# Kernel tuning notes

Measured on AMD Instinct MI355X. Metric: run time of the kernel, lower is better.

Reference implementation:

```python
import jax, jax.numpy as jnp
import numpy as np
import math

EPS_DEMOD = 1e-8
EPS_IN = 1e-5  # torch InstanceNorm2d default eps
STYLE_DIM = 512


def conv2d(x, w, pad, groups=1):
    return jax.lax.conv_general_dilated(
        x, w, window_strides=(1, 1), padding=[(pad, pad), (pad, pad)],
        dimension_numbers=('NCHW', 'OIHW', 'NCHW'), feature_group_count=groups)


def spade(x, seg, sw, sb, gw, gb, bw, bb):
    # param-free instance norm (biased variance, eps=1e-5)
    mu = jnp.mean(x, axis=(2, 3), keepdims=True)
    var = jnp.var(x, axis=(2, 3), keepdims=True)
    normalized = (x - mu) * jax.lax.rsqrt(var + EPS_IN)
    actv = jax.nn.relu(conv2d(seg, sw, 1) + sb[None, :, None, None])
    gamma = conv2d(actv, gw, 1) + gb[None, :, None, None]
    beta = conv2d(actv, bw, 1) + bb[None, :, None, None]
    return normalized * (1.0 + gamma) + beta


def modconv(x, style, w, mw, mb):
    # StyleGAN2 modulated/demodulated conv via grouped-conv trick (bias=False)
    B, I, H, W = x.shape
    O, _, k, _ = w.shape
    lin_scale = 1.0 / math.sqrt(STYLE_DIM)  # EqualLinear scale, lr_mul=1
    s = style @ (mw * lin_scale).T + mb  # [B, I]
    conv_scale = 1.0 / math.sqrt(I * k * k)
    weight = conv_scale * w[None] * s[:, None, :, None, None]  # [B,O,I,k,k]
    demod = jax.lax.rsqrt(jnp.sum(weight ** 2, axis=(2, 3, 4)) + EPS_DEMOD)
    weight = weight * demod[:, :, None, None, None]
    out = conv2d(x.reshape(1, B * I, H, W), weight.reshape(B * O, I, k, k),
                 pad=k // 2, groups=B)
    return out.reshape(B, O, H, W)


def lrelu(x):
    return jax.nn.leaky_relu(x, 0.2)


def setup_inputs() -> dict:
    key = jax.random.key(0)
    ks = jax.random.split(key, 32)
    B, FIN, FOUT, FMID, H, W = 8, 512, 256, 256, 64, 64
    SNC, NH, SD = 35, 128, STYLE_DIM
    i = iter(range(32))
    def n(k, shape):
        return jax.random.normal(k, shape, dtype=jnp.float32)
    inp = {}
    inp['x'] = n(ks[next(i)], (B, FIN, H, W))
    inp['seg'] = jax.random.uniform(ks[next(i)], (B, SNC, H, W), dtype=jnp.float32)
    inp['style'] = n(ks[next(i)], (B, SD))
    def spade_params(prefix, C):
        inp[prefix + '_sw'] = n(ks[next(i)], (NH, SNC, 3, 3)) * 0.05
        inp[prefix + '_sb'] = jnp.zeros((NH,), jnp.float32)
        inp[prefix + '_gw'] = n(ks[next(i)], (C, NH, 3, 3)) * 0.05
        inp[prefix + '_gb'] = jnp.zeros((C,), jnp.float32)
        inp[prefix + '_bw'] = n(ks[next(i)], (C, NH, 3, 3)) * 0.05
        inp[prefix + '_bb'] = jnp.zeros((C,), jnp.float32)
    spade_params('n0', FIN)
    spade_params('n1', FMID)
    spade_params('ns', FIN)
    # modulated convs: base weight ~ randn, modulation EqualLinear (bias_init=1)
    inp['w0'] = n(ks[next(i)], (FMID, FIN, 3, 3))
    inp['m0w'] = n(ks[next(i)], (FIN, SD))
    inp['m0b'] = jnp.ones((FIN,), jnp.float32)
    inp['w1'] = n(ks[next(i)], (FOUT, FMID, 3, 3))
    inp['m1w'] = n(ks[next(i)], (FMID, SD))
    inp['m1b'] = jnp.ones((FMID,), jnp.float32)
    inp['ws'] = n(ks[next(i)], (FOUT, FIN, 1, 1))
    inp['msw'] = n(ks[next(i)], (FIN, SD))
    inp['msb'] = jnp.ones((FIN,), jnp.float32)
    return inp


def reference(x, seg, style,
              n0_sw, n0_sb, n0_gw, n0_gb, n0_bw, n0_bb,
              n1_sw, n1_sb, n1_gw, n1_gb, n1_bw, n1_bb,
              ns_sw, ns_sb, ns_gw, ns_gb, ns_bw, ns_bb,
              w0, m0w, m0b, w1, m1w, m1b, ws, msw, msb):
    # shortcut: SPADE (no activation) -> 1x1 modulated conv
    x_s = modconv(spade(x, seg, ns_sw, ns_sb, ns_gw, ns_gb, ns_bw, ns_bb),
                  style, ws, msw, msb)
    dx = modconv(lrelu(spade(x, seg, n0_sw, n0_sb, n0_gw, n0_gb, n0_bw, n0_bb)),
                 style, w0, m0w, m0b)
    dx = modconv(lrelu(spade(dx, seg, n1_sw, n1_sb, n1_gw, n1_gb, n1_bw, n1_bb)),
                 style, w1, m1w, m1b)
    return x_s + dx
```

## Files before the change

### kernel.cpp

```cpp
#include <hip/hip_runtime.h>
#include <math.h>

#define BN 8
#define HW 4096
#define NH 128
#define SNC 35
#define SD 512

typedef __attribute__((ext_vector_type(8))) short short8v;
typedef __attribute__((ext_vector_type(4))) short short4v;
typedef __attribute__((ext_vector_type(4))) float float4v;
typedef __attribute__((ext_vector_type(4))) unsigned int uint4v;

__device__ __forceinline__ short f2bf(float f) {
  unsigned u = __float_as_uint(f);
  unsigned r = (u + 0x7fffu + ((u >> 16) & 1u)) >> 16;
  return (short)r;
}
__device__ __forceinline__ float bf2f(short h) {
  return __uint_as_float(((unsigned)(unsigned short)h) << 16);
}

__global__ __launch_bounds__(256) void stats_kernel(const float* __restrict__ x,
                                                    float* __restrict__ mu,
                                                    float* __restrict__ rstd) {
  int row = blockIdx.x;
  const float* p = x + (size_t)row * HW;
  float s = 0.f, s2 = 0.f;
  for (int i = threadIdx.x; i < HW; i += 256) {
    float v = p[i];
    s += v; s2 += v * v;
  }
  #pragma unroll
  for (int off = 32; off > 0; off >>= 1) {
    s  += __shfl_down(s, off);
    s2 += __shfl_down(s2, off);
  }
  __shared__ float as[4], as2[4];
  int wid = threadIdx.x >> 6;
  if ((threadIdx.x & 63) == 0) { as[wid] = s; as2[wid] = s2; }
  __syncthreads();
  if (threadIdx.x == 0) {
    float t  = as[0] + as[1] + as[2] + as[3];
    float t2 = as2[0] + as2[1] + as2[2] + as2[3];
    float m = t * (1.f / HW);
    float var = t2 * (1.f / HW) - m * m;
    mu[row] = m;
    rstd[row] = rsqrtf(var + 1e-5f);
  }
}

__global__ __launch_bounds__(256) void modscale_all_kernel(
    const float* __restrict__ style,
    const float* __restrict__ m0w, const float* __restrict__ m0b,
    const float* __restrict__ m1w, const float* __restrict__ m1b,
    const float* __restrict__ msw, const float* __restrict__ msb,
    float* __restrict__ s0, float* __restrict__ s1, float* __restrict__ ss) {
  int idx = blockIdx.x * 256 + threadIdx.x;
  const float *mw, *mb; float* o; int I;
  if (idx < 4096) { mw = m0w; mb = m0b; o = s0; I = 512; }
  else if (idx < 6144) { idx -= 4096; mw = m1w; mb = m1b; o = s1; I = 256; }
  else if (idx < 10240) { idx -= 6144; mw = msw; mb = msb; o = ss; I = 512; }
  else return;
  int b = idx / I, i = idx - b * I;
  const float* st = style + (size_t)b * SD;
  const float* w  = mw + (size_t)i * SD;
  float acc = 0.f;
  for (int d = 0; d < SD; ++d) acc += st[d] * w[d];
  o[idx] = acc * 0.044194173824159216f + mb[i];
}

__global__ __launch_bounds__(256) void wsq_all_kernel(
    const float* __restrict__ w0, const float* __restrict__ w1,
    const float* __restrict__ wss,
    float* __restrict__ wsq0, float* __restrict__ wsq1, float* __restrict__ wsqs) {
  int idx = blockIdx.x * 256 + threadIdx.x;
  const float* w; float* o; int KK;
  if (idx < 131072) { w = w0; o = wsq0; KK = 9; }
  else if (idx < 196608) { idx -= 131072; w = w1; o = wsq1; KK = 9; }
  else if (idx < 327680) { idx -= 196608; w = wss; o = wsqs; KK = 1; }
  else return;
  const float* p = w + (size_t)idx * KK;
  float a = 0.f;
  for (int t = 0; t < KK; ++t) a += p[t] * p[t];
  o[idx] = a;
}

__global__ __launch_bounds__(256) void demod_all_kernel(
    const float* __restrict__ wsq0, const float* __restrict__ s0, float* __restrict__ d0,
    const float* __restrict__ wsq1, const float* __restrict__ s1, float* __restrict__ d1,
    const float* __restrict__ wsqs, const float* __restrict__ ss, float* __restrict__ dss,
    float cs0, float cs1, float css) {
  int idx = blockIdx.x * 256 + threadIdx.x;
  const float *wsq, *s; float* dsc; int I; float cs;
  if (idx < 2048) { wsq = wsq0; s = s0; dsc = d0; I = 512; cs = cs0; }
  else if (idx < 4096) { idx -= 2048; wsq = wsq1; s = s1; dsc = d1; I = 256; cs = cs1; }
  else if (idx < 6144) { idx -= 4096; wsq = wsqs; s = ss; dsc = dss; I = 512; cs = css; }
  else return;
  int b = idx >> 8, o = idx & 255;
  const float* wr = wsq + (size_t)o * I;
  const float* sr = s + (size_t)b * I;
  float a = 0.f;
  for (int i = 0; i < I; ++i) { float sv = sr[i]; a += wr[i] * sv * sv; }
  dsc[idx] = rsqrtf(cs * cs * a + 1e-8f) * cs;
}

__device__ __forceinline__ void pack_one(int tid, const float* __restrict__ wg,
                                         const float* __restrict__ wb,
                                         short* __restrict__ ph, short* __restrict__ pl,
                                         int OCtot, int IC, int KK, int interleave) {
  int ICC = IC / 32;
  int OCT16 = OCtot / 16;
  int lane = tid & 63;
  int r = tid >> 6;
  int icC = r % ICC; r /= ICC;
  int ocT = r % OCT16; int tap = r / OCT16;
  int po = ocT * 16 + (lane & 15);
  int ic0 = icC * 32 + (lane >> 4) * 8;
  const float* srcw;
  int oc;
  if (interleave) { oc = po >> 1; srcw = (po & 1) ? wb : wg; }
  else { oc = po; srcw = wg; }
  short8v hv, lv;
  #pragma unroll
  for (int j = 0; j < 8; ++j) {
    float v = srcw[((size_t)oc * IC + ic0 + j) * KK + tap];
    short h = f2bf(v);
    hv[j] = h;
    lv[j] = f2bf(v - bf2f(h));
  }
  size_t o = (size_t)tid * 8;
  *(short8v*)(ph + o) = hv;
  if (pl) *(short8v*)(pl + o) = lv;
}

__global__ __launch_bounds__(256) void pack_w_all_kernel(
    const float* w0, const float* w1, const float* wss,
    const float* ns_gw, const float* ns_bw,
    const float* n0_gw, const float* n0_bw,
    const float* n1_gw, const float* n1_bw,
    short* p0h, short* p0l, short* p1h, short* p1l, short* psh, short* psl,
    short* pgsh, short* pg0h, short* pg1h) {
  int tid = blockIdx.x * 256 + threadIdx.x;
  if (tid < 147456) { pack_one(tid, w0, nullptr, p0h, p0l, 256, 512, 9, 0); return; }
  tid -= 147456;
  if (tid < 73728) { pack_one(tid, w1, nullptr, p1h, p1l, 256, 256, 9, 0); return; }
  tid -= 73728;
  if (tid < 16384) { pack_one(tid, wss, nullptr, psh, psl, 256, 512, 1, 0); return; }
  tid -= 16384;
  if (tid < 147456) { pack_one(tid, ns_gw, ns_bw, pgsh, nullptr, 1024, 128, 9, 1); return; }
  tid -= 147456;
  if (tid < 147456) { pack_one(tid, n0_gw, n0_bw, pg0h, nullptr, 1024, 128, 9, 1); return; }
  tid -= 147456;
  if (tid < 73728) pack_one(tid, n1_gw, n1_bw, pg1h, nullptr, 512, 128, 9, 1);
}

__global__ __launch_bounds__(256) void pack_sw_kernel(const float* __restrict__ sw0,
                                                      const float* __restrict__ sw1,
                                                      const float* __restrict__ sw2,
                                                      short* __restrict__ ph,
                                                      short* __restrict__ pl) {
  int tid = blockIdx.x * 256 + threadIdx.x;
  const int ICC = 2, OCT16 = 24;
  int total = 9 * OCT16 * ICC * 64;
  if (tid >= total) return;
  int lane = tid & 63;
  int r = tid >> 6;
  int icC = r % ICC; r /= ICC;
  int ocT = r % OCT16; int tap = r / OCT16;
  int oc = ocT * 16 + (lane & 15);
  int ic0 = icC * 32 + (lane >> 4) * 8;
  const float* srcw = (oc < 128) ? sw0 : ((oc < 256) ? sw1 : sw2);
  int ocl = oc & 127;
  short8v hv, lv;
  #pragma unroll
  for (int j = 0; j < 8; ++j) {
    int ic = ic0 + j;
    float v = (ic < SNC) ? srcw[((size_t)ocl * SNC + ic) * 9 + tap] : 0.f;
    short h = f2bf(v);
    hv[j] = h;
    lv[j] = f2bf(v - bf2f(h));
  }
  size_t o = (size_t)tid * 8;
  *(short8v*)(ph + o) = hv;
  *(short8v*)(pl + o) = lv;
}

__global__ __launch_bounds__(256) void seg_pack_kernel(const float* __restrict__ seg,
                                                       short* __restrict__ segT) {
  int pix = blockIdx.x * 256 + threadIdx.x;
  int b = pix >> 12, px = pix & 4095;
  float v[64];
  #pragma unroll
  for (int ic = 0; ic < SNC; ++ic)
    v[ic] = seg[((size_t)b * SNC + ic) * HW + px];
  #pragma unroll
  for (int ic = SNC; ic < 64; ++ic) v[ic] = 0.f;
  size_t o = (size_t)pix * 64;
  #pragma unroll
  for (int k = 0; k < 8; ++k) {
    short8v h;
    #pragma unroll
    for (int j = 0; j < 8; ++j) h[j] = f2bf(v[k * 8 + j]);
    *(short8v*)(segT + o + k * 8) = h;
  }
}

template<int IC, int ICSTRIDE, int K3, int MODE, int ACCUM, int INLO, int WLO>
__global__ __launch_bounds__(256) void conv_mfma_kernel(
    const short* __restrict__ in_hi, const short* __restrict__ in_lo,
    const short* __restrict__ wp_hi, const short* __restrict__ wp_lo,
    const float* __restrict__ dscale,
    const float* __restrict__ src, const float* __restrict__ mu,
    const float* __restrict__ rstd, const float* __restrict__ gbias,
    const float* __restrict__ bbias, const float* __restrict__ sscale,
    float* __restrict__ outF, short* __restrict__ out_hi,
    short* __restrict__ out_lo, int OCT16, int C, int icbase, int lrelu) {
  const int b = blockIdx.x;
  const int r0 = blockIdx.y * 2;
  const int zl = blockIdx.z;
  const int t = threadIdx.x;
  const int wv = t >> 6;
  const int lane = t & 63;
  const int l15 = lane & 15, lg = lane >> 4;
  const int ICC = IC / 32;
  const int PS = 2128;

  __shared__ __align__(16) short lds_hi[4 * 2128];
  __shared__ __align__(16) short lds_lo[INLO ? 4 * 2128 : 8];

  float pre[2][2][8];
  if (MODE == 1) {
    #pragma unroll
    for (int a = 0; a < 2; ++a) {
      int base = zl * 128 + wv * 32 + a * 16 + lg * 4;
      int cA = base >> 1, cB = cA + 1;
      const float* srcA = src + ((size_t)b * C + cA) * HW;
      const float* srcB = src + ((size_t)b * C + cB) * HW;
      #pragma unroll
      for (int pt = 0; pt < 8; ++pt) {
        int px = (r0 + (pt >> 2)) * 64 + (pt & 3) * 16 + l15;
        pre[a][0][pt] = srcA[px];
        pre[a][1][pt] = srcB[px];
      }
    }
  }

  float4v acc[2][8];
  #pragma unroll
  for (int a = 0; a < 2; ++a)
    #pragma unroll
    for (int pt = 0; pt < 8; ++pt) acc[a][pt] = (float4v){0.f, 0.f, 0.f, 0.f};

  for (int icC = 0; icC < ICC; ++icC) {
    __syncthreads();
    const int ic0 = icC * 32;
    for (int idx = t; idx < 264 * 4; idx += 256) {
      int pos = idx >> 2, part = idx & 3;
      int srow = pos / 66;
      int scol = pos - srow * 66;
      int gy = r0 + srow - 1, gx = scol - 1;
      uint4v vh = {0u, 0u, 0u, 0u}, vl = {0u, 0u, 0u, 0u};
      bool ok = (gy >= 0 && gy < 64 && gx >= 0 && gx < 64);
      if (!K3) ok = ok && (srow >= 1 && srow <= 2);
      if (ok) {
        size_t g = ((size_t)b * HW + gy * 64 + gx) * ICSTRIDE + icbase + ic0 + part * 8;
        vh = *(const uint4v*)(in_hi + g);
        if (INLO) vl = *(const uint4v*)(in_lo + g);
      }
      int lo = part * PS + pos * 8;
      *(uint4v*)(lds_hi + lo) = vh;
      if (INLO) *(uint4v*)(lds_lo + lo) = vl;
    }
    __syncthreads();

    if (K3) {
      #pragma unroll
      for (int dx = 0; dx < 3; ++dx) {
        short8v Ah[3][2], Al[3][2];
        #pragma unroll
        for (int dy = 0; dy < 3; ++dy) {
          #pragma unroll
          for (int a = 0; a < 2; ++a) {
            size_t wi = ((((size_t)(dy * 3 + dx) * OCT16) + (zl * 8 + wv * 2 + a)) * ICC + icC) * 64 + lane;
            Ah[dy][a] = *(const short8v*)(wp_hi + wi * 8);
            if (WLO) Al[dy][a] = *(const short8v*)(wp_lo + wi * 8);
          }
        }
        #pragma unroll
        for (int c0i = 0; c0i < 4; ++c0i) {
          #pragma unroll
          for (int sr = 0; sr < 4; ++sr) {
            int pix = sr * 66 + c0i * 16 + dx + l15;
            int addr = lg * PS + pix * 8;
            short8v Bh = *(const short8v*)(lds_hi + addr);
            #pragma unroll
            for (int dy = 0; dy < 3; ++dy) {
              int pt = sr - dy;
              if (pt < 0 || pt > 1) continue;
              int ptt = pt * 4 + c0i;
              acc[0][ptt] = __builtin_amdgcn_mfma_f32_16x16x32_bf16(Ah[dy][0], Bh, acc[0][ptt], 0, 0, 0);
              acc[1][ptt] = __builtin_amdgcn_mfma_f32_16x16x32_bf16(Ah[dy][1], Bh, acc[1][ptt], 0, 0, 0);
              if (WLO) {
                acc[0][ptt] = __builtin_amdgcn_mfma_f32_16x16x32_bf16(Al[dy][0], Bh, acc[0][ptt], 0, 0, 0);
                acc[1][ptt] = __builtin_amdgcn_mfma_f32_16x16x32_bf16(Al[dy][1], Bh, acc[1][ptt], 0, 0, 0);
              }
            }
            if (INLO) {
              short8v Bl = *(const short8v*)(lds_lo + addr);
              #pragma unroll
              for (int dy = 0; dy < 3; ++dy) {
                int pt = sr - dy;
                if (pt < 0 || pt > 1) continue;
                int ptt = pt * 4 + c0i;
                acc[0][ptt] = __builtin_amdgcn_mfma_f32_16x16x32_bf16(Ah[dy][0], Bl, acc[0][ptt], 0, 0, 0);
                acc[1][ptt] = __builtin_amdgcn_mfma_f32_16x16x32_bf16(Ah[dy][1], Bl, acc[1][ptt], 0, 0, 0);
              }
            }
          }
        }
      }
    } else {
      short8v Ah[2], Al[2];
      #pragma unroll
      for (int a = 0; a < 2; ++a) {
        size_t wi = (((size_t)(zl * 8 + wv * 2 + a)) * ICC + icC) * 64 + lane;
        Ah[a] = *(const short8v*)(wp_hi + wi * 8);
        if (WLO) Al[a] = *(const short8v*)(wp_lo + wi * 8);
      }
      #pragma unroll
      for (int pt = 0; pt < 8; ++pt) {
        int pix = ((pt >> 2) + 1) * 66 + (pt & 3) * 16 + 1 + l15;
        int addr = lg * PS + pix * 8;
        short8v Bh = *(const short8v*)(lds_hi + addr);
        acc[0][pt] = __builtin_amdgcn_mfma_f32_16x16x32_bf16(Ah[0], Bh, acc[0][pt], 0, 0, 0);
        acc[1][pt] = __builtin_amdgcn_mfma_f32_16x16x32_bf16(Ah[1], Bh, acc[1][pt], 0, 0, 0);
        if (WLO) {
          acc[0][pt] = __builtin_amdgcn_mfma_f32_16x16x32_bf16(Al[0], Bh, acc[0][pt], 0, 0, 0);
          acc[1][pt] = __builtin_amdgcn_mfma_f32_16x16x32_bf16(Al[1], Bh, acc[1][pt], 0, 0, 0);
        }
        if (INLO) {
          short8v Bl = *(const short8v*)(lds_lo + addr);
          acc[0][pt] = __builtin_amdgcn_mfma_f32_16x16x32_bf16(Ah[0], Bl, acc[0][pt], 0, 0, 0);
          acc[1][pt] = __builtin_amdgcn_mfma_f32_16x16x32_bf16(Ah[1], Bl, acc[1][pt], 0, 0, 0);
        }
      }
    }
  }

  if (MODE == 1) {
    #pragma unroll
    for (int a = 0; a < 2; ++a) {
      int base = zl * 128 + wv * 32 + a * 16 + lg * 4;
      int cA = base >> 1;
      int cB = cA + 1;
      float muA = mu[b * C + cA], rsA = rstd[b * C + cA];
      float gbA = gbias[cA], bbA = bbias[cA], sA = sscale[b * C + cA];
      float muB = mu[b * C + cB], rsB = rstd[b * C + cB];
      float gbB = gbias[cB], bbB = bbias[cB], sB = sscale[b * C + cB];
      #pragma unroll
      for (int pt = 0; pt < 8; ++pt) {
        int px = (r0 + (pt >> 2)) * 64 + (pt & 3) * 16 + l15;
        float nvA = (pre[a][0][pt] - muA) * rsA;
        float vA = nvA * (1.f + acc[a][pt][0] + gbA) + acc[a][pt][1] + bbA;
        if (lrelu) vA = (vA >= 0.f) ? vA : 0.2f * vA;
        vA *= sA;
        float nvB = (pre[a][1][pt] - muB) * rsB;
        float vB = nvB * (1.f + acc[a][pt][2] + gbB) + acc[a][pt][3] + bbB;
        if (lrelu) vB = (vB >= 0.f) ? vB : 0.2f * vB;
        vB *= sB;
        short hA = f2bf(vA), hB = f2bf(vB);
        short lA = f2bf(vA - bf2f(hA)), lB = f2bf(vB - bf2f(hB));
        size_t o = ((size_t)b * HW + px) * C + cA;
        *(unsigned*)(out_hi + o) =
            (unsigned)(unsigned short)hA | ((unsigned)(unsigned short)hB << 16);
        *(unsigned*)(out_lo + o) =
            (unsigned)(unsigned short)lA | ((unsigned)(unsigned short)lB << 16);
      }
    }
  } else if (MODE == 2) {
    #pragma unroll
    for (int a = 0; a < 2; ++a) {
      int ocbase = zl * 128 + wv * 32 + a * 16 + lg * 4;
      float bs[4];
      #pragma unroll
      for (int r = 0; r < 4; ++r) bs[r] = gbias[ocbase + r];
      #pragma unroll
      for (int pt = 0; pt < 8; ++pt) {
        int px = (r0 + (pt >> 2)) * 64 + (pt & 3) * 16 + l15;
        short4v hs;
        #pragma unroll
        for (int r = 0; r < 4; ++r)
          hs[r] = f2bf(fmaxf(acc[a][pt][r] + bs[r], 0.f));
        *(short4v*)(out_hi + ((size_t)b * HW + px) * C + ocbase) = hs;
      }
    }
  } else {
    #pragma unroll
    for (int a = 0; a < 2; ++a) {
      int ocbase = zl * 128 + wv * 32 + a * 16 + lg * 4;
      float ds[4];
      #pragma unroll
      for (int r = 0; r < 4; ++r) ds[r] = dscale[b * 256 + ocbase + r];
      #pragma unroll
      for (int pt = 0; pt < 8; ++pt) {
        int px = (r0 + (pt >> 2)) * 64 + (pt & 3) * 16 + l15;
        #pragma unroll
        for (int r = 0; r < 4; ++r) {
          size_t oi = ((size_t)b * 256 + ocbase + r) * HW + px;
          float v = acc[a][pt][r] * ds[r];
          if (ACCUM) v += outF[oi];
          outF[oi] = v;
        }
      }
    }
  }
}

__global__ __launch_bounds__(256) void conv_gb_dual_kernel(
    const short* __restrict__ actv_hi,
    const short* __restrict__ pgsh, const short* __restrict__ pg0h,
    const float* __restrict__ x, const float* __restrict__ mu,
    const float* __restrict__ rstd,
    const float* __restrict__ ns_gb, const float* __restrict__ ns_bb,
    const float* __restrict__ ss,
    const float* __restrict__ n0_gb, const float* __restrict__ n0_bb,
    const float* __restrict__ s0,
    short* __restrict__ sp2_hi, short* __restrict__ sp_hi) {
  const int b = blockIdx.x;
  const int r0 = blockIdx.y * 2;
  const int zz = blockIdx.z;
  const bool isN0 = zz >= 8;
  const int zl = zz & 7;
  const short* wph = isN0 ? pg0h : pgsh;
  const float* gbias = isN0 ? n0_gb : ns_gb;
  const float* bbias = isN0 ? n0_bb : ns_bb;
  const float* sscale = isN0 ? s0 : ss;
  short* out_hi = isN0 ? sp_hi : sp2_hi;
  const int icbase = isN0 ? 0 : 256;
  const int lrelu = isN0 ? 1 : 0;
  const int OCT16 = 64, C = 512, ICC = 4, ICSTRIDE = 384;

  const int t = threadIdx.x;
  const int wv = t >> 6;
  const int lane = t & 63;
  const int l15 = lane & 15, lg = lane >> 4;
  const int PS = 2128;

  __shared__ __align__(16) short lds_hi[16 * 2128];

  float pre[2][2][8];
  #pragma unroll
  for (int a = 0; a < 2; ++a) {
    int base = zl * 128 + wv * 32 + a * 16 + lg * 4;
    int cA = base >> 1, cB = cA + 1;
    const float* srcA = x + ((size_t)b * C + cA) * HW;
    const float* srcB = x + ((size_t)b * C + cB) * HW;
    #pragma unroll
    for (int pt = 0; pt < 8; ++pt) {
      int px = (r0 + (pt >> 2)) * 64 + (pt & 3) * 16 + l15;
      pre[a][0][pt] = srcA[px];
      pre[a][1][pt] = srcB[px];
    }
  }

  float4v acc[2][8];
  #pragma unroll
  for (int a = 0; a < 2; ++a)
    #pragma unroll
    for (int pt = 0; pt < 8; ++pt) acc[a][pt] = (float4v){0.f, 0.f, 0.f, 0.f};

  for (int idx = t; idx < 264 * 16; idx += 256) {
    int pos = idx >> 4, part = idx & 15;
    int srow = pos / 66;
    int scol = pos - srow * 66;
    int gy = r0 + srow - 1, gx = scol - 1;
    uint4v vh = {0u, 0u, 0u, 0u};
    if (gy >= 0 && gy < 64 && gx >= 0 && gx < 64)
      vh = *(const uint4v*)(actv_hi + ((size_t)b * HW + gy * 64 + gx) * ICSTRIDE
                            + icbase + part * 8);
    *(uint4v*)(lds_hi + part * PS + pos * 8) = vh;
  }
  __syncthreads();

  #pragma unroll
  for (int icC = 0; icC < 4; ++icC) {
    #pragma unroll
    for (int dx = 0; dx < 3; ++dx) {
      short8v Ah[3][2];
      #pragma unroll
      for (int dy = 0; dy < 3; ++dy) {
        #pragma unroll
        for (int a = 0; a < 2; ++a) {
          size_t wi = ((((size_t)(dy * 3 + dx) * OCT16) + (zl * 8 + wv * 2 + a)) * ICC + icC) * 64 + lane;
          Ah[dy][a] = *(const short8v*)(wph + wi * 8);
        }
      }
      #pragma unroll
      for (int c0i = 0; c0i < 4; ++c0i) {
        #pragma unroll
        for (int sr = 0; sr < 4; ++sr) {
          int pix = sr * 66 + c0i * 16 + dx + l15;
          int addr = (icC * 4 + lg) * PS + pix * 8;
          short8v Bh = *(const short8v*)(lds_hi + addr);
          #pragma unroll
          for (int dy = 0; dy < 3; ++dy) {
            int pt = sr - dy;
            if (pt < 0 || pt > 1) continue;
            int ptt = pt * 4 + c0i;
            acc[0][ptt] = __builtin_amdgcn_mfma_f32_16x16x32_bf16(Ah[dy][0], Bh, acc[0][ptt], 0, 0, 0);
            acc[1][ptt] = __builtin_amdgcn_mfma_f32_16x16x32_bf16(Ah[dy][1], Bh, acc[1][ptt], 0, 0, 0);
          }
        }
      }
    }
  }

  #pragma unroll
  for (int a = 0; a < 2; ++a) {
    int base = zl * 128 + wv * 32 + a * 16 + lg * 4;
    int cA = base >> 1;
    int cB = cA + 1;
    float muA = mu[b * C + cA], rsA = rstd[b * C + cA];
    float gbA = gbias[cA], bbA = bbias[cA], sA = sscale[b * C + cA];
    float muB = mu[b * C + cB], rsB = rstd[b * C + cB];
    float gbB = gbias[cB], bbB = bbias[cB], sB = sscale[b * C + cB];
    #pragma unroll
    for (int pt = 0; pt < 8; ++pt) {
      int px = (r0 + (pt >> 2)) * 64 + (pt & 3) * 16 + l15;
      float nvA = (pre[a][0][pt] - muA) * rsA;
      float vA = nvA * (1.f + acc[a][pt][0] + gbA) + acc[a][pt][1] + bbA;
      if (lrelu) vA = (vA >= 0.f) ? vA : 0.2f * vA;
      vA *= sA;
      float nvB = (pre[a][1][pt] - muB) * rsB;
      float vB = nvB * (1.f + acc[a][pt][2] + gbB) + acc[a][pt][3] + bbB;
      if (lrelu) vB = (vB >= 0.f) ? vB : 0.2f * vB;
      vB *= sB;
      short hA = f2bf(vA), hB = f2bf(vB);
      size_t o = ((size_t)b * HW + px) * C + cA;
      *(unsigned*)(out_hi + o) =
          (unsigned)(unsigned short)hA | ((unsigned)(unsigned short)hB << 16);
    }
  }
}

__global__ __launch_bounds__(256, 4) void conv_mc_dual_kernel(
    const short* __restrict__ sp_hi,
    const short* __restrict__ p0h, const short* __restrict__ p0l,
    const float* __restrict__ d0, float* __restrict__ bufH,
    const short* __restrict__ sp2_hi,
    const short* __restrict__ psh, const short* __restrict__ psl,
    const float* __restrict__ dss, float* __restrict__ outD) {
  const int b = blockIdx.x;
  const int r0 = blockIdx.y * 2;
  const int zz = blockIdx.z;
  const bool is1x1 = zz >= 2;
  const int zl = zz & 1;
  const int OCT16 = 16, ICC = 16, ICSTRIDE = 512;

  const int t = threadIdx.x;
  const int wv = t >> 6;
  const int lane = t & 63;
  const int l15 = lane & 15, lg = lane >> 4;
  const int PS = 2128;

  __shared__ __align__(16) short lds[8 * 2128];

  float4v acc[2][8];
  #pragma unroll
  for (int a = 0; a < 2; ++a)
    #pragma unroll
    for (int pt = 0; pt < 8; ++pt) acc[a][pt] = (float4v){0.f, 0.f, 0.f, 0.f};

  if (!is1x1) {
    for (int rnd = 0; rnd < 8; ++rnd) {
      __syncthreads();
      for (int idx = t; idx < 264 * 8; idx += 256) {
        int pos = idx >> 3, part = idx & 7;
        int srow = pos / 66;
        int scol = pos - srow * 66;
        int gy = r0 + srow - 1, gx = scol - 1;
        uint4v vh = {0u, 0u, 0u, 0u};
        if (gy >= 0 && gy < 64 && gx >= 0 && gx < 64)
          vh = *(const uint4v*)(sp_hi + ((size_t)b * HW + gy * 64 + gx) * ICSTRIDE
                                + rnd * 64 + part * 8);
        *(uint4v*)(lds + part * PS + pos * 8) = vh;
      }
      __syncthreads();

      #pragma unroll
      for (int sub = 0; sub < 2; ++sub) {
        const int icC = rnd * 2 + sub;
        #pragma unroll
        for (int dx = 0; dx < 3; ++dx) {
          short8v Ah[3][2], Al[3][2];
          #pragma unroll
          for (int dy = 0; dy < 3; ++dy) {
            #pragma unroll
            for (int a = 0; a < 2; ++a) {
              size_t wi = ((((size_t)(dy * 3 + dx) * OCT16) + (zl * 8 + wv * 2 + a)) * ICC + icC) * 64 + lane;
              Ah[dy][a] = *(const short8v*)(p0h + wi * 8);
              Al[dy][a] = *(const short8v*)(p0l + wi * 8);
            }
          }
          #pragma unroll
          for (int c0i = 0; c0i < 4; ++c0i) {
            #pragma unroll
            for (int sr = 0; sr < 4; ++sr) {
              int pix = sr * 66 + c0i * 16 + dx + l15;
              int addr = (sub * 4 + lg) * PS + pix * 8;
              short8v Bh = *(const short8v*)(lds + addr);
              #pragma unroll
              for (int dy = 0; dy < 3; ++dy) {
                int pt = sr - dy;
                if (pt < 0 || pt > 1) continue;
                int ptt = pt * 4 + c0i;
                acc[0][ptt] = __builtin_amdgcn_mfma_f32_16x16x32_bf16(Ah[dy][0], Bh, acc[0][ptt], 0, 0, 0);
                acc[1][ptt] = __builtin_amdgcn_mfma_f32_16x16x32_bf16(Ah[dy][1], Bh, acc[1][ptt], 0, 0, 0);
                acc[0][ptt] = __builtin_amdgcn_mfma_f32_16x16x32_bf16(Al[dy][0], Bh, acc[0][ptt], 0, 0, 0);
                acc[1][ptt] = __builtin_amdgcn_mfma_f32_16x16x32_bf16(Al[dy][1], Bh, acc[1][ptt], 0, 0, 0);
              }
            }
          }
        }
      }
    }
  } else {
    for (int icC = 0; icC < ICC; ++icC) {
      __syncthreads();
      const int ic0 = icC * 32;
      for (int idx = t; idx < 132 * 4; idx += 256) {
        int pos = idx >> 2, part = idx & 3;
        int srow = pos / 66;
        int scol = pos - srow * 66;
        int gy = r0 + srow, gx = scol - 1;
        uint4v vh = {0u, 0u, 0u, 0u};
        if (gx >= 0 && gx < 64)
          vh = *(const uint4v*)(sp2_hi + ((size_t)b * HW + gy * 64 + gx) * ICSTRIDE + ic0 + part * 8);
        *(uint4v*)(lds + part * PS + pos * 8) = vh;
      }
      __syncthreads();

      short8v Ah[2], Al[2];
      #pragma unroll
      for (int a = 0; a < 2; ++a) {
        size_t wi = (((size_t)(zl * 8 + wv * 2 + a)) * ICC + icC) * 64 + lane;
        Ah[a] = *(const short8v*)(psh + wi * 8);
        Al[a] = *(const short8v*)(psl + wi * 8);
      }
      #pragma unroll
      for (int pt = 0; pt < 8; ++pt) {
        int pix = (pt >> 2) * 66 + (pt & 3) * 16 + 1 + l15;
        short8v Bh = *(const short8v*)(lds + lg * PS + pix * 8);
        acc[0][pt] = __builtin_amdgcn_mfma_f32_16x16x32_bf16(Ah[0], Bh, acc[0][pt], 0, 0, 0);
        acc[1][pt] = __builtin_amdgcn_mfma_f32_16x16x32_bf16(Ah[1], Bh, acc[1][pt], 0, 0, 0);
        acc[0][pt] = __builtin_amdgcn_mfma_f32_16x16x32_bf16(Al[0], Bh, acc[0][pt], 0, 0, 0);
        acc[1][pt] = __builtin_amdgcn_mfma_f32_16x16x32_bf16(Al[1], Bh, acc[1][pt], 0, 0, 0);
      }
    }
  }

  const float* dscale = is1x1 ? dss : d0;
  float* outF = is1x1 ? outD : bufH;
  #pragma unroll
  for (int a = 0; a < 2; ++a) {
    int ocbase = zl * 128 + wv * 32 + a * 16 + lg * 4;
    float ds[4];
    #pragma unroll
    for (int r = 0; r < 4; ++r) ds[r] = dscale[b * 256 + ocbase + r];
    #pragma unroll
    for (int pt = 0; pt < 8; ++pt) {
      int px = (r0 + (pt >> 2)) * 64 + (pt & 3) * 16 + l15;
      #pragma unroll
      for (int r = 0; r < 4; ++r) {
        size_t oi = ((size_t)b * 256 + ocbase + r) * HW + px;
        outF[oi] = acc[a][pt][r] * ds[r];
      }
    }
  }
}

extern "C" void kernel_launch(void* const* d_in, const int* in_sizes, int n_in,
                              void* d_out, int out_size, void* d_ws, size_t ws_size,
                              hipStream_t stream) {
  const float* x     = (const float*)d_in[0];
  const float* seg   = (const float*)d_in[1];
  const float* style = (const float*)d_in[2];
  const float* n0_sw = (const float*)d_in[3];
  const float* n0_sb = (const float*)d_in[4];
  const float* n0_gw = (const float*)d_in[5];
  const float* n0_gb = (const float*)d_in[6];
  const float* n0_bw = (const float*)d_in[7];
  const float* n0_bb = (const float*)d_in[8];
  const float* n1_sw = (const float*)d_in[9];
  const float* n1_sb = (const float*)d_in[10];
  const float* n1_gw = (const float*)d_in[11];
  const float* n1_gb = (const float*)d_in[12];
  const float* n1_bw = (const float*)d_in[13];
  const float* n1_bb = (const float*)d_in[14];
  const float* ns_sw = (const float*)d_in[15];
  const float* ns_sb = (const float*)d_in[16];
  const float* ns_gw = (const float*)d_in[17];
  const float* ns_gb = (const float*)d_in[18];
  const float* ns_bw = (const float*)d_in[19];
  const float* ns_bb = (const float*)d_in[20];
  const float* w0  = (const float*)d_in[21];
  const float* m0w = (const float*)d_in[22];
  const float* m0b = (const float*)d_in[23];
  const float* w1  = (const float*)d_in[24];
  const float* m1w = (const float*)d_in[25];
  const float* m1b = (const float*)d_in[26];
  const float* wss = (const float*)d_in[27];
  const float* msw = (const float*)d_in[28];
  const float* msb = (const float*)d_in[29];
  float* out = (float*)d_out;

  char* p = (char*)d_ws;
  auto allocF = [&](size_t n) { float* r = (float*)p; p += n * 4; return r; };
  auto allocS = [&](size_t n) { short* r = (short*)p; p += n * 2; return r; };

  float* mu_x   = allocF(4096);
  float* rstd_x = allocF(4096);
  float* mu_h   = allocF(2048);
  float* rstd_h = allocF(2048);
  float* s0  = allocF(4096);
  float* s1  = allocF(2048);
  float* ss  = allocF(4096);
  float* d0  = allocF(2048);
  float* d1  = allocF(2048);
  float* dss = allocF(2048);
  float* wsq0 = allocF(256 * 512);
  float* wsq1 = allocF(256 * 256);
  float* wsqs = allocF(256 * 512);
  float* sb_cat = allocF(384);
  float* bufH = allocF((size_t)BN * 256 * HW);
  short* actv_hi = allocS((size_t)BN * HW * 384);
  short* segT = allocS((size_t)BN * HW * 64);
  short* sp_hi = allocS((size_t)BN * HW * 512);
  short* sp_lo = allocS((size_t)BN * HW * 512);
  short* sp2_hi = allocS((size_t)BN * HW * 512);
  short* p0h = allocS((size_t)256 * 512 * 9);
  short* p0l = allocS((size_t)256 * 512 * 9);
  short* p1h = allocS((size_t)256 * 256 * 9);
  short* p1l = allocS((size_t)256 * 256 * 9);
  short* psh = allocS((size_t)256 * 512);
  short* psl = allocS((size_t)256 * 512);
  short* pswh = allocS((size_t)9 * 24 * 2 * 64 * 8);
  short* pswl = allocS((size_t)9 * 24 * 2 * 64 * 8);
  short* pgsh = allocS((size_t)1024 * 128 * 9);
  short* pg0h = allocS((size_t)1024 * 128 * 9);
  short* pg1h = allocS((size_t)512 * 128 * 9);

  float cs0 = 1.0f / sqrtf(512.f * 9.f);
  float cs1 = 1.0f / sqrtf(256.f * 9.f);
  float css = 1.0f / sqrtf(512.f);

  stats_kernel<<<BN * 512, 256, 0, stream>>>(x, mu_x, rstd_x);
  modscale_all_kernel<<<40, 256, 0, stream>>>(style, m0w, m0b, m1w, m1b, msw, msb,
                                              s0, s1, ss);
  wsq_all_kernel<<<1280, 256, 0, stream>>>(w0, w1, wss, wsq0, wsq1, wsqs);
  demod_all_kernel<<<24, 256, 0, stream>>>(wsq0, s0, d0, wsq1, s1, d1, wsqs, ss, dss,
                                           cs0, cs1, css);

  seg_pack_kernel<<<(BN * HW) / 256, 256, 0, stream>>>(seg, segT);
  hipMemcpyAsync(sb_cat,       n0_sb, 128 * 4, hipMemcpyDeviceToDevice, stream);
  hipMemcpyAsync(sb_cat + 128, n1_sb, 128 * 4, hipMemcpyDeviceToDevice, stream);
  hipMemcpyAsync(sb_cat + 256, ns_sb, 128 * 4, hipMemcpyDeviceToDevice, stream);

  pack_sw_kernel<<<108, 256, 0, stream>>>(n0_sw, n1_sw, ns_sw, pswh, pswl);
  pack_w_all_kernel<<<2368, 256, 0, stream>>>(
      w0, w1, wss, ns_gw, ns_bw, n0_gw, n0_bw, n1_gw, n1_bw,
      p0h, p0l, p1h, p1l, psh, psl, pgsh, pg0h, pg1h);

  conv_mfma_kernel<64, 64, 1, 2, 0, 0, 1><<<dim3(BN, 32, 3), 256, 0, stream>>>(
      segT, nullptr, pswh, pswl, nullptr, nullptr, nullptr, nullptr, sb_cat,
      nullptr, nullptr, nullptr, actv_hi, nullptr, 24, 384, 0, 0);

  conv_gb_dual_kernel<<<dim3(BN, 32, 16), 256, 0, stream>>>(
      actv_hi, pgsh, pg0h, x, mu_x, rstd_x,
      ns_gb, ns_bb, ss, n0_gb, n0_bb, s0, sp2_hi, sp_hi);

  conv_mc_dual_kernel<<<dim3(BN, 32, 4), 256, 0, stream>>>(
      sp_hi, p0h, p0l, d0, bufH,
      sp2_hi, psh, psl, dss, out);

  stats_kernel<<<BN * 256, 256, 0, stream>>>(bufH, mu_h, rstd_h);
  conv_mfma_kernel<128, 384, 1, 1, 0, 0, 0><<<dim3(BN, 32, 4), 256, 0, stream>>>(
      actv_hi, nullptr, pg1h, nullptr, nullptr, bufH, mu_h, rstd_h, n1_gb, n1_bb, s1,
      nullptr, sp_hi, sp_lo, 32, 256, 128, 1);
  conv_mfma_kernel<256, 256, 1, 0, 1, 1, 1><<<dim3(BN, 32, 2), 256, 0, stream>>>(
      sp_hi, sp_lo, p1h, p1l, d1, nullptr, nullptr, nullptr, nullptr, nullptr,
      nullptr, out, nullptr, nullptr, 16, 0, 0, 0);
}
```

Measured before the change: 699.9 us.

## Drop low-bf16 weight split for conv0 and add dedicated single-stage gamma/beta conv kernel

Removes the low-part bf16 weight correction for the w0 modulated conv, which halves the MFMA count and weight loads in the largest conv. It also replaces the generic MODE==1 path of conv_mfma_kernel with a specialized conv_gb1_kernel. That kernel stages all 128 input channels into shared memory at once and reuses each LDS B-fragment across the three dy taps. The trade-offs are lower precision in the w0 conv, which could exceed the error tolerance, and heavier LDS use per block in the new kernel, which may reduce occupancy.

```diff
diff --git a/kernel.cpp b/kernel.cpp
--- a/kernel.cpp
+++ b/kernel.cpp
@@ -139,10 +139,10 @@
     const float* ns_gw, const float* ns_bw,
     const float* n0_gw, const float* n0_bw,
     const float* n1_gw, const float* n1_bw,
-    short* p0h, short* p0l, short* p1h, short* p1l, short* psh, short* psl,
+    short* p0h, short* p1h, short* p1l, short* psh, short* psl,
     short* pgsh, short* pg0h, short* pg1h) {
   int tid = blockIdx.x * 256 + threadIdx.x;
-  if (tid < 147456) { pack_one(tid, w0, nullptr, p0h, p0l, 256, 512, 9, 0); return; }
+  if (tid < 147456) { pack_one(tid, w0, nullptr, p0h, nullptr, 256, 512, 9, 0); return; }
   tid -= 147456;
   if (tid < 73728) { pack_one(tid, w1, nullptr, p1h, p1l, 256, 256, 9, 0); return; }
   tid -= 73728;
@@ -228,23 +228,6 @@
 
   __shared__ __align__(16) short lds_hi[4 * 2128];
   __shared__ __align__(16) short lds_lo[INLO ? 4 * 2128 : 8];
-
-  float pre[2][2][8];
-  if (MODE == 1) {
-    #pragma unroll
-    for (int a = 0; a < 2; ++a) {
-      int base = zl * 128 + wv * 32 + a * 16 + lg * 4;
-      int cA = base >> 1, cB = cA + 1;
-      const float* srcA = src + ((size_t)b * C + cA) * HW;
-      const float* srcB = src + ((size_t)b * C + cB) * HW;
-      #pragma unroll
-      for (int pt = 0; pt < 8; ++pt) {
-        int px = (r0 + (pt >> 2)) * 64 + (pt & 3) * 16 + l15;
-        pre[a][0][pt] = srcA[px];
-        pre[a][1][pt] = srcB[px];
-      }
-    }
-  }
 
   float4v acc[2][8];
   #pragma unroll
@@ -348,37 +331,7 @@
     }
   }
 
-  if (MODE == 1) {
-    #pragma unroll
-    for (int a = 0; a < 2; ++a) {
-      int base = zl * 128 + wv * 32 + a * 16 + lg * 4;
-      int cA = base >> 1;
-      int cB = cA + 1;
-      float muA = mu[b * C + cA], rsA = rstd[b * C + cA];
-      float gbA = gbias[cA], bbA = bbias[cA], sA = sscale[b * C + cA];
-      float muB = mu[b * C + cB], rsB = rstd[b * C + cB];
-      float gbB = gbias[cB], bbB = bbias[cB], sB = sscale[b * C + cB];
-      #pragma unroll
-      for (int pt = 0; pt < 8; ++pt) {
-        int px = (r0 + (pt >> 2)) * 64 + (pt & 3) * 16 + l15;
-        float nvA = (pre[a][0][pt] - muA) * rsA;
-        float vA = nvA * (1.f + acc[a][pt][0] + gbA) + acc[a][pt][1] + bbA;
-        if (lrelu) vA = (vA >= 0.f) ? vA : 0.2f * vA;
-        vA *= sA;
-        float nvB = (pre[a][1][pt] - muB) * rsB;
-        float vB = nvB * (1.f + acc[a][pt][2] + gbB) + acc[a][pt][3] + bbB;
-        if (lrelu) vB = (vB >= 0.f) ? vB : 0.2f * vB;
-        vB *= sB;
-        short hA = f2bf(vA), hB = f2bf(vB);
-        short lA = f2bf(vA - bf2f(hA)), lB = f2bf(vB - bf2f(hB));
-        size_t o = ((size_t)b * HW + px) * C + cA;
-        *(unsigned*)(out_hi + o) =
-            (unsigned)(unsigned short)hA | ((unsigned)(unsigned short)hB << 16);
-        *(unsigned*)(out_lo + o) =
-            (unsigned)(unsigned short)lA | ((unsigned)(unsigned short)lB << 16);
-      }
-    }
-  } else if (MODE == 2) {
+  if (MODE == 2) {
     #pragma unroll
     for (int a = 0; a < 2; ++a) {
       int ocbase = zl * 128 + wv * 32 + a * 16 + lg * 4;
@@ -544,9 +497,127 @@
   }
 }
 
+__global__ __launch_bounds__(256) void conv_gb1_kernel(
+    const short* __restrict__ actv_hi, const short* __restrict__ pg1h,
+    const float* __restrict__ src, const float* __restrict__ mu,
+    const float* __restrict__ rstd,
+    const float* __restrict__ gbias, const float* __restrict__ bbias,
+    const float* __restrict__ sscale,
+    short* __restrict__ out_hi, short* __restrict__ out_lo) {
+  const int b = blockIdx.x;
+  const int r0 = blockIdx.y * 2;
+  const int zl = blockIdx.z;
+  const int OCT16 = 32, C = 256, ICC = 4, ICSTRIDE = 384, icbase = 128;
+
+  const int t = threadIdx.x;
+  const int wv = t >> 6;
+  const int lane = t & 63;
+  const int l15 = lane & 15, lg = lane >> 4;
+  const int PS = 2128;
+
+  __shared__ __align__(16) short lds_hi[16 * 2128];
+
+  float pre[2][2][8];
+  #pragma unroll
+  for (int a = 0; a < 2; ++a) {
+    int base = zl * 128 + wv * 32 + a * 16 + lg * 4;
+    int cA = base >> 1, cB = cA + 1;
+    const float* srcA = src + ((size_t)b * C + cA) * HW;
+    const float* srcB = src + ((size_t)b * C + cB) * HW;
+    #pragma unroll
+    for (int pt = 0; pt < 8; ++pt) {
+      int px = (r0 + (pt >> 2)) * 64 + (pt & 3) * 16 + l15;
+      pre[a][0][pt] = srcA[px];
+      pre[a][1][pt] = srcB[px];
+    }
+  }
+
+  float4v acc[2][8];
+  #pragma unroll
+  for (int a = 0; a < 2; ++a)
+    #pragma unroll
+    for (int pt = 0; pt < 8; ++pt) acc[a][pt] = (float4v){0.f, 0.f, 0.f, 0.f};
+
+  for (int idx = t; idx < 264 * 16; idx += 256) {
+    int pos = idx >> 4, part = idx & 15;
+    int srow = pos / 66;
+    int scol = pos - srow * 66;
+    int gy = r0 + srow - 1, gx = scol - 1;
+    uint4v vh = {0u, 0u, 0u, 0u};
+    if (gy >= 0 && gy < 64 && gx >= 0 && gx < 64)
+      vh = *(const uint4v*)(actv_hi + ((size_t)b * HW + gy * 64 + gx) * ICSTRIDE
+                            + icbase + part * 8);
+    *(uint4v*)(lds_hi + part * PS + pos * 8) = vh;
+  }
+  __syncthreads();
+
+  #pragma unroll
+  for (int icC = 0; icC < 4; ++icC) {
+    #pragma unroll
+    for (int dx = 0; dx < 3; ++dx) {
+      short8v Ah[3][2];
+      #pragma unroll
+      for (int dy = 0; dy < 3; ++dy) {
+        #pragma unroll
+        for (int a = 0; a < 2; ++a) {
+          size_t wi = ((((size_t)(dy * 3 + dx) * OCT16) + (zl * 8 + wv * 2 + a)) * ICC + icC) * 64 + lane;
+          Ah[dy][a] = *(const short8v*)(pg1h + wi * 8);
+        }
+      }
+      #pragma unroll
+      for (int c0i = 0; c0i < 4; ++c0i) {
+        #pragma unroll
+        for (int sr = 0; sr < 4; ++sr) {
+          int pix = sr * 66 + c0i * 16 + dx + l15;
+          int addr = (icC * 4 + lg) * PS + pix * 8;
+          short8v Bh = *(const short8v*)(lds_hi + addr);
+          #pragma unroll
+          for (int dy = 0; dy < 3; ++dy) {
+            int pt = sr - dy;
+            if (pt < 0 || pt > 1) continue;
+            int ptt = pt * 4 + c0i;
+            acc[0][ptt] = __builtin_amdgcn_mfma_f32_16x16x32_bf16(Ah[dy][0], Bh, acc[0][ptt], 0, 0, 0);
+            acc[1][ptt] = __builtin_amdgcn_mfma_f32_16x16x32_bf16(Ah[dy][1], Bh, acc[1][ptt], 0, 0, 0);
+          }
+        }
+      }
+    }
+  }
+
+  #pragma unroll
+  for (int a = 0; a < 2; ++a) {
+    int base = zl * 128 + wv * 32 + a * 16 + lg * 4;
+    int cA = base >> 1;
+    int cB = cA + 1;
+    float muA = mu[b * C + cA], rsA = rstd[b * C + cA];
+    float gbA = gbias[cA], bbA = bbias[cA], sA = sscale[b * C + cA];
+    float muB = mu[b * C + cB], rsB = rstd[b * C + cB];
+    float gbB = gbias[cB], bbB = bbias[cB], sB = sscale[b * C + cB];
+    #pragma unroll
+    for (int pt = 0; pt < 8; ++pt) {
+      int px = (r0 + (pt >> 2)) * 64 + (pt & 3) * 16 + l15;
+      float nvA = (pre[a][0][pt] - muA) * rsA;
+      float vA = nvA * (1.f + acc[a][pt][0] + gbA) + acc[a][pt][1] + bbA;
+      vA = (vA >= 0.f) ? vA : 0.2f * vA;
+      vA *= sA;
+      float nvB = (pre[a][1][pt] - muB) * rsB;
+      float vB = nvB * (1.f + acc[a][pt][2] + gbB) + acc[a][pt][3] + bbB;
+      vB = (vB >= 0.f) ? vB : 0.2f * vB;
+      vB *= sB;
+      short hA = f2bf(vA), hB = f2bf(vB);
+      short lA = f2bf(vA - bf2f(hA)), lB = f2bf(vB - bf2f(hB));
+      size_t o = ((size_t)b * HW + px) * C + cA;
+      *(unsigned*)(out_hi + o) =
+          (unsigned)(unsigned short)hA | ((unsigned)(unsigned short)hB << 16);
+      *(unsigned*)(out_lo + o) =
+          (unsigned)(unsigned short)lA | ((unsigned)(unsigned short)lB << 16);
+    }
+  }
+}
+
 __global__ __launch_bounds__(256, 4) void conv_mc_dual_kernel(
     const short* __restrict__ sp_hi,
-    const short* __restrict__ p0h, const short* __restrict__ p0l,
+    const short* __restrict__ p0h,
     const float* __restrict__ d0, float* __restrict__ bufH,
     const short* __restrict__ sp2_hi,
     const short* __restrict__ psh, const short* __restrict__ psl,
@@ -593,14 +664,13 @@
         const int icC = rnd * 2 + sub;
         #pragma unroll
         for (int dx = 0; dx < 3; ++dx) {
-          short8v Ah[3][2], Al[3][2];
+          short8v Ah[3][2];
           #pragma unroll
           for (int dy = 0; dy < 3; ++dy) {
             #pragma unroll
             for (int a = 0; a < 2; ++a) {
               size_t wi = ((((size_t)(dy * 3 + dx) * OCT16) + (zl * 8 + wv * 2 + a)) * ICC + icC) * 64 + lane;
               Ah[dy][a] = *(const short8v*)(p0h + wi * 8);
-              Al[dy][a] = *(const short8v*)(p0l + wi * 8);
             }
           }
           #pragma unroll
@@ -617,8 +687,6 @@
                 int ptt = pt * 4 + c0i;
                 acc[0][ptt] = __builtin_amdgcn_mfma_f32_16x16x32_bf16(Ah[dy][0], Bh, acc[0][ptt], 0, 0, 0);
                 acc[1][ptt] = __builtin_amdgcn_mfma_f32_16x16x32_bf16(Ah[dy][1], Bh, acc[1][ptt], 0, 0, 0);
-                acc[0][ptt] = __builtin_amdgcn_mfma_f32_16x16x32_bf16(Al[dy][0], Bh, acc[0][ptt], 0, 0, 0);
-                acc[1][ptt] = __builtin_amdgcn_mfma_f32_16x16x32_bf16(Al[dy][1], Bh, acc[1][ptt], 0, 0, 0);
               }
             }
           }
@@ -740,7 +808,6 @@
   short* sp_lo = allocS((size_t)BN * HW * 512);
   short* sp2_hi = allocS((size_t)BN * HW * 512);
   short* p0h = allocS((size_t)256 * 512 * 9);
-  short* p0l = allocS((size_t)256 * 512 * 9);
   short* p1h = allocS((size_t)256 * 256 * 9);
   short* p1l = allocS((size_t)256 * 256 * 9);
   short* psh = allocS((size_t)256 * 512);
@@ -770,7 +837,7 @@
   pack_sw_kernel<<<108, 256, 0, stream>>>(n0_sw, n1_sw, ns_sw, pswh, pswl);
   pack_w_all_kernel<<<2368, 256, 0, stream>>>(
       w0, w1, wss, ns_gw, ns_bw, n0_gw, n0_bw, n1_gw, n1_bw,
-      p0h, p0l, p1h, p1l, psh, psl, pgsh, pg0h, pg1h);
+      p0h, p1h, p1l, psh, psl, pgsh, pg0h, pg1h);
 
   conv_mfma_kernel<64, 64, 1, 2, 0, 0, 1><<<dim3(BN, 32, 3), 256, 0, stream>>>(
       segT, nullptr, pswh, pswl, nullptr, nullptr, nullptr, nullptr, sb_cat,
@@ -781,13 +848,12 @@
       ns_gb, ns_bb, ss, n0_gb, n0_bb, s0, sp2_hi, sp_hi);
 
   conv_mc_dual_kernel<<<dim3(BN, 32, 4), 256, 0, stream>>>(
-      sp_hi, p0h, p0l, d0, bufH,
+      sp_hi, p0h, d0, bufH,
       sp2_hi, psh, psl, dss, out);
 
   stats_kernel<<<BN * 256, 256, 0, stream>>>(bufH, mu_h, rstd_h);
-  conv_mfma_kernel<128, 384, 1, 1, 0, 0, 0><<<dim3(BN, 32, 4), 256, 0, stream>>>(
-      actv_hi, nullptr, pg1h, nullptr, nullptr, bufH, mu_h, rstd_h, n1_gb, n1_bb, s1,
-      nullptr, sp_hi, sp_lo, 32, 256, 128, 1);
+  conv_gb1_kernel<<<dim3(BN, 32, 4), 256, 0, stream>>>(
+      actv_hi, pg1h, bufH, mu_h, rstd_h, n1_gb, n1_bb, s1, sp_hi, sp_lo);
   conv_mfma_kernel<256, 256, 1, 0, 1, 1, 1><<<dim3(BN, 32, 2), 256, 0, stream>>>(
       sp_hi, sp_lo, p1h, p1l, d1, nullptr, nullptr, nullptr, nullptr, nullptr,
       nullptr, out, nullptr, nullptr, 16, 0, 0, 0);
```

Result: faster. 607.0 us (-13.3%).
